# Optimization experiments

Measured on AMD Instinct MI355X. Metric: run time of the kernel, lower is better.

The kernel has to match this reference:

```python
import jax, jax.numpy as jnp
import numpy as np

B, L, D = 256, 256, 128          # batch, max_len, embedding_dim
H = W = 16                       # H=int(sqrt(L)), W=L//H
N, CBD = 128, 1024               # embedding_num, code_book_dim = N*8 = D*8
BETA = 0.25
BN_EPS = 1e-3                    # tf.layers.batch_normalization default


def _conv(x, w, b):
    return jax.lax.conv_general_dilated(x, w, (1, 1), 'VALID',
        dimension_numbers=('NHWC', 'HWIO', 'NHWC')) + b


def _convT(x, w, b):
    return jax.lax.conv_transpose(x, w, (1, 1), 'VALID',
        dimension_numbers=('NHWC', 'HWIO', 'NHWC')) + b


def _bn(x, g, b):
    # inference-mode BN with moving_mean=0, moving_var=1 (tf.layers default training=False)
    return g * (x * (1.0 / np.sqrt(1.0 + BN_EPS))) + b


def setup_inputs() -> dict:
    key = jax.random.key(0)
    ks = jax.random.split(key, 24)
    rn = lambda k, s, sc=0.05: (jax.random.normal(k, s, dtype=jnp.float32) * sc)
    inp = {
        'x': jax.random.normal(ks[0], (B, L, D), dtype=jnp.float32),
        'mask': jnp.ones((B, L), dtype=jnp.float32),
        'code_book': jax.random.normal(ks[1], (N, CBD), dtype=jnp.float32),
        # encoder: conv2d k=2 valid, channels D -> 2D -> 4D -> 8D
        'ew1': rn(ks[2], (2, 2, D, 2 * D)), 'eb1': jnp.zeros((2 * D,), jnp.float32),
        'eg1': jnp.ones((2 * D,), jnp.float32), 'ebt1': jnp.zeros((2 * D,), jnp.float32),
        'ew2': rn(ks[3], (2, 2, 2 * D, 4 * D)), 'eb2': jnp.zeros((4 * D,), jnp.float32),
        'eg2': jnp.ones((4 * D,), jnp.float32), 'ebt2': jnp.zeros((4 * D,), jnp.float32),
        'ew3': rn(ks[4], (2, 2, 4 * D, 8 * D)), 'eb3': jnp.zeros((8 * D,), jnp.float32),
        # decoder: conv2d_transpose k=2 valid, channels 8D -> 4D -> 2D -> D
        'dw1': rn(ks[5], (2, 2, 8 * D, 4 * D)), 'db1': jnp.zeros((4 * D,), jnp.float32),
        'dg1': jnp.ones((4 * D,), jnp.float32), 'dbt1': jnp.zeros((4 * D,), jnp.float32),
        'dw2': rn(ks[6], (2, 2, 4 * D, 2 * D)), 'db2': jnp.zeros((2 * D,), jnp.float32),
        'dg2': jnp.ones((2 * D,), jnp.float32), 'dbt2': jnp.zeros((2 * D,), jnp.float32),
        'dw3': rn(ks[7], (2, 2, 2 * D, D)), 'db3': jnp.zeros((D,), jnp.float32),
    }
    return inp


def reference(x, mask, code_book,
              ew1, eb1, eg1, ebt1, ew2, eb2, eg2, ebt2, ew3, eb3,
              dw1, db1, dg1, dbt1, dw2, db2, dg2, dbt2, dw3, db3):
    # ---- encoder (conv branch) ----
    xi = x.reshape(-1, H, W, D)                                   # [B,16,16,D]
    h = jax.nn.relu(_bn(_conv(xi, ew1, eb1), eg1, ebt1))          # [B,15,15,2D]
    h = jax.nn.relu(_bn(_conv(h, ew2, eb2), eg2, ebt2))           # [B,14,14,4D]
    x_encode = _conv(h, ew3, eb3)                                 # [B,13,13,8D]

    # ---- VQ codebook lookup (get_quantized) ----
    flat = x_encode.reshape(-1, CBD)                              # [B*169, CBD]
    dist = (jnp.sum(flat ** 2, axis=1, keepdims=True)
            + jnp.sum(code_book ** 2, axis=1)
            - 2.0 * flat @ code_book.T)                           # [B*169, N]
    idx = jnp.argmin(dist, axis=1)
    quantized = code_book[idx].reshape(x_encode.shape)            # gather == one_hot @ code_book

    # ---- straight-through + decoder ----
    ste = x_encode + jax.lax.stop_gradient(quantized - x_encode)
    h = jax.nn.relu(_bn(_convT(ste, dw1, db1), dg1, dbt1))        # [B,14,14,4D]
    h = jax.nn.relu(_bn(_convT(h, dw2, db2), dg2, dbt2))          # [B,15,15,2D]
    vq = _convT(h, dw3, db3)                                      # [B,16,16,D]
    vq_x = vq.reshape(-1, L, D)

    vq_mean = jnp.sum(vq_x, axis=1) / jnp.sum(mask, axis=-1, keepdims=True)

    recon = jnp.mean((x - vq_x) ** 2)
    vq_l = jnp.mean((quantized - jax.lax.stop_gradient(x_encode)) ** 2)
    commit = jnp.mean((x_encode - jax.lax.stop_gradient(quantized)) ** 2)
    vqvae_loss = recon + vq_l + BETA * commit
    return (vq_mean, vq_x, x_encode, quantized, vqvae_loss)
```

## Files before the change

### kernel.cpp

```cpp
#include <hip/hip_runtime.h>
#include <math.h>

typedef float f4 __attribute__((ext_vector_type(4)));
typedef short s8 __attribute__((ext_vector_type(8)));

#define WS_FLOATS 66000000L
__device__ float g_fallback[WS_FLOATS];

__device__ __forceinline__ f4 ldg4(const float* p) { return *(const f4*)p; }

__device__ __forceinline__ unsigned short bfr(float x) {
    unsigned int u = __float_as_uint(x);
    u += 0x7fffu + ((u >> 16) & 1u);
    return (unsigned short)(u >> 16);
}
__device__ __forceinline__ float bff(unsigned short h) {
    return __uint_as_float(((unsigned int)h) << 16);
}
__device__ __forceinline__ s8 z8() { s8 z = {0,0,0,0,0,0,0,0}; return z; }

__device__ __forceinline__ void split8(const f4& x0, const f4& x1, s8& hi, s8& lo) {
#pragma unroll
    for (int e = 0; e < 4; ++e) {
        unsigned short h0 = bfr(x0[e]);
        hi[e] = (short)h0; lo[e] = (short)bfr(x0[e] - bff(h0));
        unsigned short h1 = bfr(x1[e]);
        hi[e + 4] = (short)h1; lo[e + 4] = (short)bfr(x1[e] - bff(h1));
    }
}

__device__ __forceinline__ void tpose64(const float* __restrict__ src,
                                        short* __restrict__ hi,
                                        short* __restrict__ lo,
                                        int K, int N, int tileId, int tid)
{
    __shared__ float ld[64][65];
    const int nt = N >> 6;
    const int k0 = (tileId / nt) << 6, n0 = (tileId % nt) << 6;
#pragma unroll
    for (int i = 0; i < 16; ++i) {
        int idx = tid + (i << 8);
        int r = idx >> 6, c = idx & 63;
        ld[r][c] = src[(long)(k0 + r) * N + n0 + c];
    }
    __syncthreads();
#pragma unroll
    for (int i = 0; i < 16; ++i) {
        int idx = tid + (i << 8);
        int nr = idx >> 6, kc = idx & 63;
        float x = ld[kc][nr];
        unsigned short h = bfr(x);
        long o = (long)(n0 + nr) * K + k0 + kc;
        hi[o] = (short)h;
        if (lo) lo[o] = (short)bfr(x - bff(h));
    }
}

__global__ __launch_bounds__(256)
void tpose_all(const float* __restrict__ ew1, const float* __restrict__ ew2,
               const float* __restrict__ ew3, const float* __restrict__ dw1,
               const float* __restrict__ dw2, const float* __restrict__ dw3,
               const float* __restrict__ cb,
               short* __restrict__ ewt1h, short* __restrict__ ewt1l,
               short* __restrict__ ewt2h, short* __restrict__ ewt2l,
               short* __restrict__ ewt3h,
               short* __restrict__ dwt1Th, short* __restrict__ dwt1Tl,
               short* __restrict__ dwt2h, short* __restrict__ dwt3h,
               short* __restrict__ cbh, short* __restrict__ cbl,
               float* __restrict__ zbuf)
{
    int b = blockIdx.x, t = threadIdx.x;
    if (b < 32) {
        tpose64(ew1, ewt1h, ewt1l, 512, 256, b, t);
    } else if (b < 160) {
        tpose64(ew2, ewt2h, ewt2l, 1024, 512, b - 32, t);
    } else if (b < 672) {
        tpose64(ew3, ewt3h, nullptr, 2048, 1024, b - 160, t);
    } else if (b < 1184) {
        int r = b - 672; int tt = r >> 7; int tile = r & 127;
        tpose64(dw1 + (long)tt * 524288, dwt1Th + (long)tt * 524288,
                dwt1Tl + (long)tt * 524288, 1024, 512, tile, t);
    } else if (b < 1312) {
        tpose64(dw2, dwt2h, nullptr, 2048, 256, b - 1184, t);
    } else if (b < 1344) {
        tpose64(dw3, dwt3h, nullptr, 1024, 128, b - 1312, t);
    } else if (b < 1856) {
        int i = (b - 1344) * 256 + t;
        float x = cb[i]; unsigned short h = bfr(x);
        cbh[i] = (short)h; cbl[i] = (short)bfr(x - bff(h));
    } else {
#pragma unroll
        for (int q = 0; q < 8; ++q) zbuf[t + 256 * q] = 0.f;
    }
}

__global__ __launch_bounds__(256)
void tposeP1(const float* __restrict__ p1, short* __restrict__ hi,
             short* __restrict__ lo)
{
    tpose64(p1, hi, lo, 2048, 128, blockIdx.x, threadIdx.x);
}

template<int EPI>
__global__ __launch_bounds__(512, 2)
void gemm256(const short* __restrict__ aSrc, const short* __restrict__ wHi,
             const float* __restrict__ bias, const float* __restrict__ gamma,
             const float* __restrict__ beta, void* __restrict__ oHi,
             double* __restrict__ sacc, const short* __restrict__ zsrc,
             int IH, int IW, int OHOW, int OW, int N, int K, int off,
             int ntShift, float bns)
{
    extern __shared__ short smem[];

    const int tid = threadIdx.x;
    const int w = tid >> 6;
    const int l = tid & 63;
    const int lr = l >> 3;
    const int lc = l & 7;
    const int fr = l & 15, fq = l >> 4;
    const int wm = (w >> 2) * 128;
    const int wn = (w & 3) * 64;

    int m0, n0;
    {
        const int nwg = gridDim.x;
        const int bid = blockIdx.x;
        const int q = nwg >> 3, r = nwg & 7;
        const int xcd = bid & 7, c = bid >> 3;
        const int wg = (xcd < r ? xcd * (q + 1) : r * (q + 1) + (xcd - r) * q) + c;
        const int NTm1 = (1 << ntShift) - 1;
        m0 = (wg >> ntShift) * 256;
        n0 = (wg & NTm1) * 256;
    }

    int bOff[4], oiA[4], ojA[4], bRowB[4];
#pragma unroll
    for (int i = 0; i < 4; ++i) {
        int row = (w << 5) + (i << 3) + lr;
        int m = m0 + row;
        int b = m / OHOW; int rem = m - b * OHOW;
        oiA[i] = rem / OW; ojA[i] = rem - oiA[i] * OW;
        bOff[i] = b * IH * IW;
        bRowB[i] = (n0 + row) * K;
    }
    const int swz = (lc ^ lr) << 3;

    auto stage = [&](int sel, int kc) {
        short* Ab = smem + sel * 16384;
        short* Bb = smem + 32768 + sel * 16384;
        const int t = kc >> 9;
        const int ci = (kc & 511) + swz;
        const int di = (t >> 1) + off, dj = (t & 1) + off;
#pragma unroll
        for (int i = 0; i < 4; ++i) {
            int ii = oiA[i] + di, jj = ojA[i] + dj;
            bool v = (ii >= 0) && (ii < IH) && (jj >= 0) && (jj < IW);
            const short* sA = v ? aSrc + (long)(bOff[i] + ii * IW + jj) * 512 + ci
                                : zsrc + (l << 3);
            __builtin_amdgcn_global_load_lds(
                (const __attribute__((address_space(1))) void*)sA,
                (__attribute__((address_space(3))) void*)(Ab + (((w << 5) + (i << 3)) * 64)),
                16, 0, 0);
            const short* sB = wHi + bRowB[i] + kc + swz;
            __builtin_amdgcn_global_load_lds(
                (const __attribute__((address_space(1))) void*)sB,
                (__attribute__((address_space(3))) void*)(Bb + (((w << 5) + (i << 3)) * 64)),
                16, 0, 0);
        }
    };

    f4 acc[8][4];
#pragma unroll
    for (int a = 0; a < 8; ++a)
#pragma unroll
        for (int b = 0; b < 4; ++b) acc[a][b] = (f4){0.f, 0.f, 0.f, 0.f};

    const int NT = K >> 6;
    stage(0, 0);
    stage(1, 64);

    for (int t = 0; t < NT; ++t) {
        const int sel = t & 1;
        const short* Ab = smem + sel * 16384;
        const short* Bb = smem + 32768 + sel * 16384;

        if (t < NT - 1) asm volatile("s_waitcnt vmcnt(8)" ::: "memory");
        else            asm volatile("s_waitcnt vmcnt(0)" ::: "memory");
        __builtin_amdgcn_s_barrier();
        __builtin_amdgcn_sched_barrier(0);

        s8 af[8], bf[4];
#pragma unroll
        for (int mf = 0; mf < 8; ++mf) {
            int row = wm + mf * 16 + fr;
            int c = fq ^ (row & 7);
            af[mf] = *(const s8*)&Ab[row * 64 + (c << 3)];
        }
#pragma unroll
        for (int nf = 0; nf < 4; ++nf) {
            int row = wn + nf * 16 + fr;
            int c = fq ^ (row & 7);
            bf[nf] = *(const s8*)&Bb[row * 64 + (c << 3)];
        }
        asm volatile("s_waitcnt lgkmcnt(0)" ::: "memory");
        __builtin_amdgcn_sched_barrier(0);
        __builtin_amdgcn_s_setprio(1);
#pragma unroll
        for (int mf = 0; mf < 8; ++mf)
#pragma unroll
            for (int nf = 0; nf < 4; ++nf)
                acc[mf][nf] = __builtin_amdgcn_mfma_f32_16x16x32_bf16(
                    af[mf], bf[nf], acc[mf][nf], 0, 0, 0);
        __builtin_amdgcn_s_setprio(0);

#pragma unroll
        for (int mf = 0; mf < 8; ++mf) {
            int row = wm + mf * 16 + fr;
            int c = (4 + fq) ^ (row & 7);
            af[mf] = *(const s8*)&Ab[row * 64 + (c << 3)];
        }
#pragma unroll
        for (int nf = 0; nf < 4; ++nf) {
            int row = wn + nf * 16 + fr;
            int c = (4 + fq) ^ (row & 7);
            bf[nf] = *(const s8*)&Bb[row * 64 + (c << 3)];
        }
        asm volatile("s_waitcnt lgkmcnt(0)" ::: "memory");
        __builtin_amdgcn_sched_barrier(0);
        __builtin_amdgcn_s_barrier();
        __builtin_amdgcn_sched_barrier(0);
        if (t + 2 < NT) stage(sel, (t + 2) << 6);

        __builtin_amdgcn_s_setprio(1);
#pragma unroll
        for (int mf = 0; mf < 8; ++mf)
#pragma unroll
            for (int nf = 0; nf < 4; ++nf)
                acc[mf][nf] = __builtin_amdgcn_mfma_f32_16x16x32_bf16(
                    af[mf], bf[nf], acc[mf][nf], 0, 0, 0);
        __builtin_amdgcn_s_setprio(0);
    }

    if (EPI == 3) {
        float bi[4];
#pragma unroll
        for (int nf = 0; nf < 4; ++nf) bi[nf] = bias[n0 + wn + nf * 16 + fr];
        double tsum = 0.0;
#pragma unroll
        for (int mf = 0; mf < 8; ++mf)
#pragma unroll
            for (int j = 0; j < 4; ++j) {
                long gm = m0 + wm + mf * 16 + fq * 4 + j;
                float* orow = (float*)oHi + gm * (long)N + n0;
#pragma unroll
                for (int nf = 0; nf < 4; ++nf) {
                    float v = acc[mf][nf][j] + bi[nf];
                    orow[wn + nf * 16 + fr] = v;
                    tsum += (double)v * v;
                }
            }
        __syncthreads();
        double* rd = (double*)smem;
        rd[tid] = tsum; __syncthreads();
        for (int h = 256; h; h >>= 1) {
            if (tid < h) rd[tid] += rd[tid + h];
            __syncthreads();
        }
        if (tid == 0) atomicAdd(sacc, rd[0]);
    } else {
        float bi[4], ga[4], be[4];
#pragma unroll
        for (int nf = 0; nf < 4; ++nf) {
            int col = n0 + wn + nf * 16 + fr;
            bi[nf] = bias[col]; ga[nf] = gamma[col]; be[nf] = beta[col];
        }
#pragma unroll
        for (int mf = 0; mf < 8; ++mf)
#pragma unroll
            for (int j = 0; j < 4; ++j) {
                long gm = m0 + wm + mf * 16 + fq * 4 + j;
                short* orow = (short*)oHi + gm * (long)N + n0;
#pragma unroll
                for (int nf = 0; nf < 4; ++nf) {
                    float v = ga[nf] * ((acc[mf][nf][j] + bi[nf]) * bns) + be[nf];
                    orow[wn + nf * 16 + fr] = (short)bfr(fmaxf(v, 0.f));
                }
            }
    }
}

template<int SPLIT, int ASRC, int EPI, int OUTF>
__global__ __launch_bounds__(256, 2)
void mfma_conv(const void* __restrict__ aHi, const void* __restrict__ aLo,
               const short* __restrict__ wHi, const short* __restrict__ wLo,
               const float* __restrict__ bias, const float* __restrict__ gamma,
               const float* __restrict__ beta,
               void* __restrict__ oHi, void* __restrict__ oLo,
               int* __restrict__ idxo,
               const float* __restrict__ xref, float* __restrict__ colsum,
               double* __restrict__ sacc,
               int IH, int IW, int Cin, int cinShift, int OHOW, int OW,
               int N, int K, int off, int ntShift, float bns)
{
    constexpr int PL = 128 * 64;
    constexpr int NPL = (SPLIT == 1) ? 3 : 4;
    __shared__ short smem[NPL * PL];
    short* Ah = smem;
    short* Al  = smem + PL;
    short* BhS = smem + 2 * PL;
    short* BlS = smem + 3 * PL;

    const int tid = threadIdx.x;
    const int lane = tid & 63, wid = tid >> 6;
    const int fr = lane & 15, fq = lane >> 4;
    const int wm = (wid >> 1) * 64, wn = (wid & 1) * 64;

    int m0, n0;
    {
        const int nwg = gridDim.x;
        const int bid = blockIdx.x;
        const int q = nwg >> 3, r = nwg & 7;
        const int xcd = bid & 7, c = bid >> 3;
        const int wg = (xcd < r ? xcd * (q + 1) : r * (q + 1) + (xcd - r) * q) + c;
        const int NTm1 = (1 << ntShift) - 1;
        m0 = (wg >> ntShift) * 128;
        n0 = (wg & NTm1) * 128;
    }

    const int sr = tid >> 1;
    const int skh = (tid & 1) << 5;

    long tapOff[4]; bool tv[4];
    {
        int m = m0 + sr;
        int b = m / OHOW; int rem = m - b * OHOW;
        int oi = rem / OW; int oj = rem - oi * OW;
#pragma unroll
        for (int t = 0; t < 4; ++t) {
            int ii = oi + (t >> 1) + off, jj = oj + (t & 1) + off;
            bool v = (ii >= 0) && (ii < IH) && (jj >= 0) && (jj < IW);
            tv[t] = v;
            tapOff[t] = ((long)b * IH + (v ? ii : 0)) * IW + (v ? jj : 0);
        }
    }

    f4 acc[4][4];
#pragma unroll
    for (int a = 0; a < 4; ++a)
#pragma unroll
        for (int b = 0; b < 4; ++b) acc[a][b] = (f4){0.f, 0.f, 0.f, 0.f};

    const short* wHrow = wHi + (long)(n0 + sr) * K;
    const short* wLrow = (SPLIT == 2) ? (wLo + (long)(n0 + sr) * K) : nullptr;

    const int swzW = (sr & 7) << 3;
    const int sbase = sr * 64;

    s8 rah[4], ral[4], rbh[4], rbl[4];
    f4 rax0[4], rax1[4];

    auto LOADREGS = [&](int kc) {
        const int kk = kc + skh;
        const int t = kk >> cinShift;
        const int ci = kk & (Cin - 1);
        const bool v = tv[t];
        if (ASRC == 0) {
            const float* p = (const float*)aHi + tapOff[t] * Cin + ci;
#pragma unroll
            for (int q = 0; q < 4; ++q) {
                rax0[q] = v ? ldg4(p + 8 * q) : (f4){0.f,0.f,0.f,0.f};
                rax1[q] = v ? ldg4(p + 8 * q + 4) : (f4){0.f,0.f,0.f,0.f};
            }
        } else if (ASRC == 1) {
            const short* ph = (const short*)aHi + tapOff[t] * Cin + ci;
            const short* pl = (const short*)aLo + tapOff[t] * Cin + ci;
#pragma unroll
            for (int q = 0; q < 4; ++q) {
                rah[q] = v ? *(const s8*)(ph + 8 * q) : z8();
                ral[q] = v ? *(const s8*)(pl + 8 * q) : z8();
            }
        } else {
            const short* ph = (const short*)aHi + tapOff[t] * Cin + ci;
#pragma unroll
            for (int q = 0; q < 4; ++q) rah[q] = v ? *(const s8*)(ph + 8 * q) : z8();
        }
        if (SPLIT == 2) {
#pragma unroll
            for (int q = 0; q < 4; ++q) {
                rbh[q] = *(const s8*)(wHrow + kc + skh + 8 * q);
                rbl[q] = *(const s8*)(wLrow + kc + skh + 8 * q);
            }
        }
    };

    auto STORE = [&]() {
        if (ASRC == 0) {
#pragma unroll
            for (int q = 0; q < 4; ++q) split8(rax0[q], rax1[q], rah[q], ral[q]);
        }
#pragma unroll
        for (int q = 0; q < 4; ++q) {
            int kx = (skh + 8 * q) ^ swzW;
            *(s8*)&Ah[sbase + kx] = rah[q];
            if (SPLIT == 2) {
                *(s8*)&Al[sbase + kx]  = ral[q];
                *(s8*)&BhS[sbase + kx] = rbh[q];
                *(s8*)&BlS[sbase + kx] = rbl[q];
            }
        }
    };

    auto stageB = [&](int bsel, int kc2) {
        short* bb = smem + (1 + bsel) * PL;
        const int rr0 = wid << 5;
#pragma unroll
        for (int i = 0; i < 4; ++i) {
            const int r = rr0 + 8 * i + (lane >> 3);
            const int c = lane & 7;
            const short* src = wHi + (long)(n0 + r) * K + kc2 + 8 * (c ^ (r & 7));
            __builtin_amdgcn_global_load_lds(
                (const __attribute__((address_space(1))) void*)src,
                (__attribute__((address_space(3))) void*)(bb + (rr0 + 8 * i) * 64),
                16, 0, 0);
        }
    };

    int bcur = 0;
    LOADREGS(0);
    if (SPLIT == 1) stageB(0, 0);

    for (int kc = 0; kc < K; kc += 64) {
        if (SPLIT == 1) {
            asm volatile("s_waitcnt lgkmcnt(0)" ::: "memory");
            __builtin_amdgcn_s_barrier();
            STORE();
            if (kc + 64 < K) {
                stageB(bcur ^ 1, kc + 64);
                asm volatile("s_waitcnt vmcnt(4)" ::: "memory");
            } else {
                asm volatile("s_waitcnt vmcnt(0)" ::: "memory");
            }
            __builtin_amdgcn_sched_barrier(0);
            asm volatile("s_waitcnt lgkmcnt(0)" ::: "memory");
            __builtin_amdgcn_s_barrier();
        } else {
            __syncthreads();
            STORE();
            __syncthreads();
        }
        if (kc + 64 < K) LOADREGS(kc + 64);

        const short* Bc = (SPLIT == 1) ? (smem + (1 + bcur) * PL) : BhS;

        __builtin_amdgcn_s_setprio(1);
#pragma unroll
        for (int ks = 0; ks < 2; ++ks) {
            const int colk = ks * 32 + fq * 8;
            s8 afh[4], afl[4], bfh[4], bfl[4];
#pragma unroll
            for (int mf = 0; mf < 4; ++mf) {
                int ar = wm + mf * 16 + fr;
                int ai = ar * 64 + (colk ^ ((ar & 7) << 3));
                afh[mf] = *(const s8*)&Ah[ai];
                if (SPLIT == 2) afl[mf] = *(const s8*)&Al[ai];
            }
#pragma unroll
            for (int nf = 0; nf < 4; ++nf) {
                int br = wn + nf * 16 + fr;
                int bi2 = br * 64 + (colk ^ ((br & 7) << 3));
                bfh[nf] = *(const s8*)&Bc[bi2];
                if (SPLIT == 2) bfl[nf] = *(const s8*)&BlS[bi2];
            }
#pragma unroll
            for (int mf = 0; mf < 4; ++mf)
#pragma unroll
                for (int nf = 0; nf < 4; ++nf) {
                    acc[mf][nf] = __builtin_amdgcn_mfma_f32_16x16x32_bf16(
                        afh[mf], bfh[nf], acc[mf][nf], 0, 0, 0);
                    if (SPLIT == 2) {
                        acc[mf][nf] = __builtin_amdgcn_mfma_f32_16x16x32_bf16(
                            afh[mf], bfl[nf], acc[mf][nf], 0, 0, 0);
                        acc[mf][nf] = __builtin_amdgcn_mfma_f32_16x16x32_bf16(
                            afl[mf], bfh[nf], acc[mf][nf], 0, 0, 0);
                    }
                }
        }
        __builtin_amdgcn_s_setprio(0);
        bcur ^= 1;
    }

    if (EPI == 2) {
        __syncthreads();
        float* pbv = (float*)smem;
        int*   piv = (int*)((float*)smem + 256);
        float cnv[4];
#pragma unroll
        for (int nf = 0; nf < 4; ++nf) cnv[nf] = bias[n0 + wn + nf * 16 + fr];
#pragma unroll
        for (int mf = 0; mf < 4; ++mf)
#pragma unroll
            for (int j = 0; j < 4; ++j) {
                float best = 3.4e38f; int bi = 0;
#pragma unroll
                for (int nf = 0; nf < 4; ++nf) {
                    float d = cnv[nf] - 2.0f * acc[mf][nf][j];
                    int col = wn + nf * 16 + fr;
                    if (d < best) { best = d; bi = col; }
                }
#pragma unroll
                for (int sh = 1; sh <= 8; sh <<= 1) {
                    float ov = __shfl_xor(best, sh, 64);
                    int ob = __shfl_xor(bi, sh, 64);
                    if (ov < best || (ov == best && ob < bi)) { best = ov; bi = ob; }
                }
                if (fr == 0) {
                    int r = wm + mf * 16 + fq * 4 + j;
                    pbv[(wid & 1) * 128 + r] = best;
                    piv[(wid & 1) * 128 + r] = bi;
                }
            }
        __syncthreads();
        double win = 0.0;
        if (tid < 128) {
            float b0 = pbv[tid], b1 = pbv[128 + tid];
            int i0 = piv[tid], i1 = piv[128 + tid];
            idxo[m0 + tid] = (b1 < b0) ? i1 : i0;
            win = (double)((b1 < b0) ? b1 : b0);
        }
        __syncthreads();
        double* rd = (double*)smem;
        rd[tid] = win; __syncthreads();
        for (int h = 128; h; h >>= 1) {
            if (tid < h) rd[tid] += rd[tid + h];
            __syncthreads();
        }
        if (tid == 0) atomicAdd(sacc, rd[0]);
        return;
    }

    float bi[4], ga[4], be[4];
#pragma unroll
    for (int nf = 0; nf < 4; ++nf) {
        int col = n0 + wn + nf * 16 + fr;
        bi[nf] = bias[col];
        if (EPI == 1) { ga[nf] = gamma[col]; be[nf] = beta[col]; }
    }
    double tsum = 0.0;
    float csum[4] = {0.f, 0.f, 0.f, 0.f};
#pragma unroll
    for (int mf = 0; mf < 4; ++mf)
#pragma unroll
        for (int j = 0; j < 4; ++j) {
            long gm = m0 + wm + mf * 16 + fq * 4 + j;
#pragma unroll
            for (int nf = 0; nf < 4; ++nf) {
                int col = n0 + wn + nf * 16 + fr;
                float vv = acc[mf][nf][j] + bi[nf];
                if (EPI == 1) {
                    vv = ga[nf] * (vv * bns) + be[nf];
                    vv = fmaxf(vv, 0.f);
                }
                long o = gm * (long)N + col;
                if (OUTF == 0) {
                    ((float*)oHi)[o] = vv;
                } else if (OUTF == 2) {
                    ((short*)oHi)[o] = (short)bfr(vv);
                } else {
                    unsigned short h = bfr(vv);
                    ((short*)oHi)[o] = (short)h;
                    ((short*)oLo)[o] = (short)bfr(vv - bff(h));
                }
                if (EPI == 3) tsum += (double)vv * vv;
                if (EPI == 4) {
                    float d = vv - xref[o];
                    tsum += (double)d * d;
                    csum[nf] += vv;
                }
            }
        }
    if (EPI == 4) {
        int bb128 = (m0 >> 8) * 128;
#pragma unroll
        for (int nf = 0; nf < 4; ++nf)
            atomicAdd(&colsum[bb128 + n0 + wn + nf * 16 + fr], csum[nf]);
    }
    if (EPI == 3 || EPI == 4) {
        __syncthreads();
        double* rd = (double*)smem;
        rd[tid] = tsum; __syncthreads();
        for (int h = 128; h; h >>= 1) {
            if (tid < h) rd[tid] += rd[tid + h];
            __syncthreads();
        }
        if (tid == 0) atomicAdd(sacc, rd[0]);
    }
}

__global__ void code_bias(const float* __restrict__ cb, const float* __restrict__ eb3,
                          float* __restrict__ bias2)
{
    int c = blockIdx.x * 4 + (threadIdx.x >> 6);
    int lane = threadIdx.x & 63;
    if (c >= 128) return;
    const f4* p = (const f4*)(cb + (long)c * 1024);
    const f4* e = (const f4*)eb3;
    float s2 = 0.f, su = 0.f;
#pragma unroll
    for (int q = 0; q < 4; ++q) {
        f4 v = p[q * 64 + lane];
        f4 w = e[q * 64 + lane];
        s2 += (v[0]*v[0] + v[1]*v[1]) + (v[2]*v[2] + v[3]*v[3]);
        su += (v[0]*w[0] + v[1]*w[1]) + (v[2]*w[2] + v[3]*w[3]);
    }
#pragma unroll
    for (int sh = 32; sh; sh >>= 1) {
        s2 += __shfl_xor(s2, sh, 64);
        su += __shfl_xor(su, sh, 64);
    }
    if (lane == 0) bias2[c] = s2 - 2.f * su;
}

__global__ __launch_bounds__(256)
void d1_gather(const float* __restrict__ CD, const int* __restrict__ idx,
               const float* __restrict__ db1, const float* __restrict__ dg1,
               const float* __restrict__ dbt1, short* __restrict__ out, float bns)
{
    int m = blockIdx.x * 4 + (threadIdx.x >> 6);
    int lane = threadIdx.x & 63;
    if (m >= 50176) return;
    int b = m / 196, rem = m - b * 196;
    int oi = rem / 14, oj = rem - oi * 14;
    float2 acc[4];
#pragma unroll
    for (int q = 0; q < 4; ++q) acc[q] = make_float2(0.f, 0.f);
#pragma unroll
    for (int t = 0; t < 4; ++t) {
        int ii = oi - 1 + (t >> 1), jj = oj - 1 + (t & 1);
        if (ii >= 0 && ii < 13 && jj >= 0 && jj < 13) {
            int c = idx[(b * 13 + ii) * 13 + jj];
            const float2* p = (const float2*)(CD + ((long)c * 2048 + t * 512));
#pragma unroll
            for (int q = 0; q < 4; ++q) {
                float2 v = p[lane + 64 * q];
                acc[q].x += v.x; acc[q].y += v.y;
            }
        }
    }
#pragma unroll
    for (int q = 0; q < 4; ++q) {
        int n = 2 * (lane + 64 * q);
        float v0 = fmaxf(dg1[n]     * ((acc[q].x + db1[n])     * bns) + dbt1[n],     0.f);
        float v1 = fmaxf(dg1[n + 1] * ((acc[q].y + db1[n + 1]) * bns) + dbt1[n + 1], 0.f);
        short2 s2v;
        s2v.x = (short)bfr(v0); s2v.y = (short)bfr(v1);
        ((short2*)out)[(long)m * 256 + lane + 64 * q] = s2v;
    }
}

__global__ void gather_rows(const float* __restrict__ cb, const int* __restrict__ idx,
                            float* __restrict__ q)
{
    int m = blockIdx.x;
    int c = idx[m];
    const f4* src = (const f4*)(cb + (long)c * 1024);
    f4* dst = (f4*)(q + (long)m * 1024);
    dst[threadIdx.x] = src[threadIdx.x];
}

__global__ void finalize2(const double* __restrict__ s, float* __restrict__ loss)
{
    if (threadIdx.x == 0)
        loss[0] = (float)(s[0] / 8388608.0 + 1.25 * ((s[1] + s[2]) / 44302336.0));
}

__global__ void vq_mean_fin(const float* __restrict__ colsum,
                            const float* __restrict__ mask, float* __restrict__ o)
{
    __shared__ float red[128];
    int b = blockIdx.x;
    int d = threadIdx.x;
    red[d] = mask[b * 256 + d] + mask[b * 256 + 128 + d];
    __syncthreads();
    for (int h = 64; h; h >>= 1) { if (d < h) red[d] += red[d + h]; __syncthreads(); }
    o[b * 128 + d] = colsum[b * 128 + d] / red[0];
}

extern "C" void kernel_launch(void* const* d_in, const int* in_sizes, int n_in,
                              void* d_out, int out_size, void* d_ws, size_t ws_size,
                              hipStream_t stream)
{
    const float* x    = (const float*)d_in[0];
    const float* mask = (const float*)d_in[1];
    const float* cb   = (const float*)d_in[2];
    const float* ew1 = (const float*)d_in[3];
    const float* eb1 = (const float*)d_in[4];
    const float* eg1 = (const float*)d_in[5];
    const float* ebt1= (const float*)d_in[6];
    const float* ew2 = (const float*)d_in[7];
    const float* eb2 = (const float*)d_in[8];
    const float* eg2 = (const float*)d_in[9];
    const float* ebt2= (const float*)d_in[10];
    const float* ew3 = (const float*)d_in[11];
    const float* eb3 = (const float*)d_in[12];
    const float* dw1 = (const float*)d_in[13];
    const float* db1 = (const float*)d_in[14];
    const float* dg1 = (const float*)d_in[15];
    const float* dbt1= (const float*)d_in[16];
    const float* dw2 = (const float*)d_in[17];
    const float* db2 = (const float*)d_in[18];
    const float* dg2 = (const float*)d_in[19];
    const float* dbt2= (const float*)d_in[20];
    const float* dw3 = (const float*)d_in[21];
    const float* db3 = (const float*)d_in[22];

    float* out = (float*)d_out;
    float* o_vqmean = out;
    float* o_vqx    = out + 32768;
    float* o_xe     = out + 8421376;
    float* o_q      = out + 52723712;
    float* o_loss   = out + 97026048;

    float* base;
    if (ws_size >= (size_t)WS_FLOATS * 4) {
        base = (float*)d_ws;
    } else {
        void* p = nullptr;
        hipGetSymbolAddress(&p, HIP_SYMBOL(g_fallback));
        base = (float*)p;
    }

    float* cur = base;
    short* h1h = (short*)cur; cur += 7372800;
    short* h1l = (short*)cur; cur += 7372800;
    short* h2h = (short*)cur; cur += 12845056;
    short* h2l = (short*)cur; cur += 12845056;
    short* d1o = (short*)cur; cur += 12845056;
    short* d2o = (short*)cur; cur += 7372800;
    short* ewt1h = (short*)cur; cur += 65536;
    short* ewt1l = (short*)cur; cur += 65536;
    short* ewt2h = (short*)cur; cur += 262144;
    short* ewt2l = (short*)cur; cur += 262144;
    short* ewt3h = (short*)cur; cur += 1048576;
    short* dwt1Th = (short*)cur; cur += 1048576;
    short* dwt1Tl = (short*)cur; cur += 1048576;
    short* dwt2h = (short*)cur; cur += 262144;
    short* dwt3h = (short*)cur; cur += 65536;
    short* cbh   = (short*)cur; cur += 65536;
    short* cbl   = (short*)cur; cur += 65536;
    float* P1raw = cur; cur += 262144;
    short* wvh   = (short*)cur; cur += 131072;
    short* wvl   = (short*)cur; cur += 131072;
    float* CDt   = cur; cur += 262144;
    float* bias2 = cur; cur += 128;
    float* zbuf  = cur; cur += 2048;
    int* idxb = (int*)cur; cur += 43264;
    float* colsum = cur; cur += 32768;
    double* sdbl = (double*)cur; cur += 16;

    const float bns = (float)(1.0 / sqrt(1.0 + 1e-3));

    hipFuncSetAttribute(reinterpret_cast<const void*>(&gemm256<3>),
                        hipFuncAttributeMaxDynamicSharedMemorySize, 131072);
    hipFuncSetAttribute(reinterpret_cast<const void*>(&gemm256<1>),
                        hipFuncAttributeMaxDynamicSharedMemorySize, 131072);

    hipMemsetAsync(colsum, 0, 32768 * sizeof(float), stream);
    hipMemsetAsync(sdbl, 0, 3 * sizeof(double), stream);
    tpose_all<<<1857, 256, 0, stream>>>(ew1, ew2, ew3, dw1, dw2, dw3, cb,
        ewt1h, ewt1l, ewt2h, ewt2l, ewt3h, dwt1Th, dwt1Tl, dwt2h, dwt3h,
        cbh, cbl, zbuf);
    code_bias<<<32, 256, 0, stream>>>(cb, eb3, bias2);

    mfma_conv<2, 0, 0, 0><<<16, 256, 0, stream>>>(
        ew3, nullptr, cbh, cbl, zbuf, nullptr, nullptr, P1raw, nullptr, nullptr,
        nullptr, nullptr, nullptr,
        2, 2050, 1024, 10, 2048, 2048, 128, 1024, 0, 0, bns);
    tposeP1<<<64, 256, 0, stream>>>(P1raw, wvh, wvl);
    mfma_conv<2, 0, 0, 0><<<16, 256, 0, stream>>>(
        cb, nullptr, dwt1Th, dwt1Tl, zbuf, nullptr, nullptr, CDt, nullptr, nullptr,
        nullptr, nullptr, nullptr,
        2, 130, 1024, 10, 128, 128, 2048, 1024, 0, 4, bns);

    mfma_conv<2, 0, 1, 1><<<900, 256, 0, stream>>>(
        x, nullptr, ewt1h, ewt1l, eb1, eg1, ebt1, h1h, h1l, nullptr,
        nullptr, nullptr, nullptr,
        16, 16, 128, 7, 225, 15, 256, 512, 0, 1, bns);
    mfma_conv<2, 1, 1, 1><<<1568, 256, 0, stream>>>(
        h1h, h1l, ewt2h, ewt2l, eb2, eg2, ebt2, h2h, h2l, nullptr,
        nullptr, nullptr, nullptr,
        15, 15, 256, 8, 196, 14, 512, 1024, 0, 2, bns);
    gemm256<3><<<676, 512, 131072, stream>>>(
        h2h, ewt3h, eb3, nullptr, nullptr, o_xe, sdbl + 1, (const short*)zbuf,
        14, 14, 169, 13, 1024, 2048, 0, 2, bns);

    mfma_conv<2, 1, 2, 0><<<338, 256, 0, stream>>>(
        h2h, h2l, wvh, wvl, bias2, nullptr, nullptr, nullptr, nullptr, idxb,
        nullptr, nullptr, sdbl + 2,
        14, 14, 512, 9, 169, 13, 128, 2048, 0, 0, bns);
    gather_rows<<<43264, 256, 0, stream>>>(cb, idxb, o_q);

    d1_gather<<<12544, 256, 0, stream>>>(CDt, idxb, db1, dg1, dbt1, d1o, bns);
    gemm256<1><<<225, 512, 131072, stream>>>(
        d1o, dwt2h, db2, dg2, dbt2, d2o, nullptr, (const short*)zbuf,
        14, 14, 225, 15, 256, 2048, -1, 0, bns);
    mfma_conv<1, 2, 4, 0><<<512, 256, 0, stream>>>(
        d2o, nullptr, dwt3h, nullptr, db3, nullptr, nullptr, o_vqx, nullptr, nullptr,
        x, colsum, sdbl + 0,
        15, 15, 256, 8, 256, 16, 128, 1024, -1, 0, bns);

    vq_mean_fin<<<256, 128, 0, stream>>>(colsum, mask, o_vqmean);
    finalize2<<<1, 64, 0, stream>>>(sdbl, o_loss);
}
```

Baseline: 883.8 us.

## Fuse codebook gather, bias, and loss finalize into neighboring kernels

```diff
diff --git a/kernel.cpp b/kernel.cpp
--- a/kernel.cpp
+++ b/kernel.cpp
@@ -60,14 +60,14 @@
 void tpose_all(const float* __restrict__ ew1, const float* __restrict__ ew2,
                const float* __restrict__ ew3, const float* __restrict__ dw1,
                const float* __restrict__ dw2, const float* __restrict__ dw3,
-               const float* __restrict__ cb,
+               const float* __restrict__ cb, const float* __restrict__ eb3,
                short* __restrict__ ewt1h, short* __restrict__ ewt1l,
                short* __restrict__ ewt2h, short* __restrict__ ewt2l,
                short* __restrict__ ewt3h,
                short* __restrict__ dwt1Th, short* __restrict__ dwt1Tl,
                short* __restrict__ dwt2h, short* __restrict__ dwt3h,
                short* __restrict__ cbh, short* __restrict__ cbl,
-               float* __restrict__ zbuf)
+               float* __restrict__ zbuf, float* __restrict__ bias2)
 {
     int b = blockIdx.x, t = threadIdx.x;
     if (b < 32) {
@@ -88,9 +88,30 @@
         int i = (b - 1344) * 256 + t;
         float x = cb[i]; unsigned short h = bfr(x);
         cbh[i] = (short)h; cbl[i] = (short)bfr(x - bff(h));
+    } else if (b < 1857) {
+#pragma unroll
+        for (int q = 0; q < 8; ++q) zbuf[t + 256 * q] = 0.f;
     } else {
-#pragma unroll
-        for (int q = 0; q < 8; ++q) zbuf[t + 256 * q] = 0.f;
+        int c = (b - 1857) * 4 + (t >> 6);
+        int lane = t & 63;
+        if (c < 128) {
+            const f4* p = (const f4*)(cb + (long)c * 1024);
+            const f4* e = (const f4*)eb3;
+            float s2 = 0.f, su = 0.f;
+#pragma unroll
+            for (int q = 0; q < 4; ++q) {
+                f4 v = p[q * 64 + lane];
+                f4 w = e[q * 64 + lane];
+                s2 += (v[0]*v[0] + v[1]*v[1]) + (v[2]*v[2] + v[3]*v[3]);
+                su += (v[0]*w[0] + v[1]*w[1]) + (v[2]*w[2] + v[3]*w[3]);
+            }
+#pragma unroll
+            for (int sh = 32; sh; sh >>= 1) {
+                s2 += __shfl_xor(s2, sh, 64);
+                su += __shfl_xor(su, sh, 64);
+            }
+            if (lane == 0) bias2[c] = s2 - 2.f * su;
+        }
     }
 }
 
@@ -493,6 +514,8 @@
         __syncthreads();
         float* pbv = (float*)smem;
         int*   piv = (int*)((float*)smem + 256);
+        int*   fidx = (int*)((float*)smem + 512);
+        double* rd = (double*)((float*)smem + 768);
         float cnv[4];
 #pragma unroll
         for (int nf = 0; nf < 4; ++nf) cnv[nf] = bias[n0 + wn + nf * 16 + fr];
@@ -524,17 +547,26 @@
         if (tid < 128) {
             float b0 = pbv[tid], b1 = pbv[128 + tid];
             int i0 = piv[tid], i1 = piv[128 + tid];
-            idxo[m0 + tid] = (b1 < b0) ? i1 : i0;
+            int sel = (b1 < b0) ? i1 : i0;
+            idxo[m0 + tid] = sel;
+            fidx[tid] = sel;
             win = (double)((b1 < b0) ? b1 : b0);
         }
         __syncthreads();
-        double* rd = (double*)smem;
         rd[tid] = win; __syncthreads();
         for (int h = 128; h; h >>= 1) {
             if (tid < h) rd[tid] += rd[tid + h];
             __syncthreads();
         }
         if (tid == 0) atomicAdd(sacc, rd[0]);
+        const float* cbf = xref;
+        float* oq = (float*)oHi;
+#pragma unroll 4
+        for (int r = 0; r < 128; ++r) {
+            int c = fidx[r];
+            f4 v = *(const f4*)&cbf[(long)c * 1024 + 4 * tid];
+            *(f4*)&oq[((long)(m0 + r)) * 1024 + 4 * tid] = v;
+        }
         return;
     }
 
@@ -596,30 +628,6 @@
     }
 }
 
-__global__ void code_bias(const float* __restrict__ cb, const float* __restrict__ eb3,
-                          float* __restrict__ bias2)
-{
-    int c = blockIdx.x * 4 + (threadIdx.x >> 6);
-    int lane = threadIdx.x & 63;
-    if (c >= 128) return;
-    const f4* p = (const f4*)(cb + (long)c * 1024);
-    const f4* e = (const f4*)eb3;
-    float s2 = 0.f, su = 0.f;
-#pragma unroll
-    for (int q = 0; q < 4; ++q) {
-        f4 v = p[q * 64 + lane];
-        f4 w = e[q * 64 + lane];
-        s2 += (v[0]*v[0] + v[1]*v[1]) + (v[2]*v[2] + v[3]*v[3]);
-        su += (v[0]*w[0] + v[1]*w[1]) + (v[2]*w[2] + v[3]*w[3]);
-    }
-#pragma unroll
-    for (int sh = 32; sh; sh >>= 1) {
-        s2 += __shfl_xor(s2, sh, 64);
-        su += __shfl_xor(su, sh, 64);
-    }
-    if (lane == 0) bias2[c] = s2 - 2.f * su;
-}
-
 __global__ __launch_bounds__(256)
 void d1_gather(const float* __restrict__ CD, const int* __restrict__ idx,
                const float* __restrict__ db1, const float* __restrict__ dg1,
@@ -657,24 +665,10 @@
     }
 }
 
-__global__ void gather_rows(const float* __restrict__ cb, const int* __restrict__ idx,
-                            float* __restrict__ q)
-{
-    int m = blockIdx.x;
-    int c = idx[m];
-    const f4* src = (const f4*)(cb + (long)c * 1024);
-    f4* dst = (f4*)(q + (long)m * 1024);
-    dst[threadIdx.x] = src[threadIdx.x];
-}
-
-__global__ void finalize2(const double* __restrict__ s, float* __restrict__ loss)
-{
-    if (threadIdx.x == 0)
-        loss[0] = (float)(s[0] / 8388608.0 + 1.25 * ((s[1] + s[2]) / 44302336.0));
-}
-
 __global__ void vq_mean_fin(const float* __restrict__ colsum,
-                            const float* __restrict__ mask, float* __restrict__ o)
+                            const float* __restrict__ mask,
+                            const double* __restrict__ s,
+                            float* __restrict__ o, float* __restrict__ loss)
 {
     __shared__ float red[128];
     int b = blockIdx.x;
@@ -683,6 +677,8 @@
     __syncthreads();
     for (int h = 64; h; h >>= 1) { if (d < h) red[d] += red[d + h]; __syncthreads(); }
     o[b * 128 + d] = colsum[b * 128 + d] / red[0];
+    if (b == 0 && d == 0)
+        loss[0] = (float)(s[0] / 8388608.0 + 1.25 * ((s[1] + s[2]) / 44302336.0));
 }
 
 extern "C" void kernel_launch(void* const* d_in, const int* in_sizes, int n_in,
@@ -766,10 +762,9 @@
 
     hipMemsetAsync(colsum, 0, 32768 * sizeof(float), stream);
     hipMemsetAsync(sdbl, 0, 3 * sizeof(double), stream);
-    tpose_all<<<1857, 256, 0, stream>>>(ew1, ew2, ew3, dw1, dw2, dw3, cb,
+    tpose_all<<<1889, 256, 0, stream>>>(ew1, ew2, ew3, dw1, dw2, dw3, cb, eb3,
         ewt1h, ewt1l, ewt2h, ewt2l, ewt3h, dwt1Th, dwt1Tl, dwt2h, dwt3h,
-        cbh, cbl, zbuf);
-    code_bias<<<32, 256, 0, stream>>>(cb, eb3, bias2);
+        cbh, cbl, zbuf, bias2);
 
     mfma_conv<2, 0, 0, 0><<<16, 256, 0, stream>>>(
         ew3, nullptr, cbh, cbl, zbuf, nullptr, nullptr, P1raw, nullptr, nullptr,
@@ -794,10 +789,9 @@
         14, 14, 169, 13, 1024, 2048, 0, 2, bns);
 
     mfma_conv<2, 1, 2, 0><<<338, 256, 0, stream>>>(
-        h2h, h2l, wvh, wvl, bias2, nullptr, nullptr, nullptr, nullptr, idxb,
-        nullptr, nullptr, sdbl + 2,
+        h2h, h2l, wvh, wvl, bias2, nullptr, nullptr, o_q, nullptr, idxb,
+        cb, nullptr, sdbl + 2,
         14, 14, 512, 9, 169, 13, 128, 2048, 0, 0, bns);
-    gather_rows<<<43264, 256, 0, stream>>>(cb, idxb, o_q);
 
     d1_gather<<<12544, 256, 0, stream>>>(CDt, idxb, db1, dg1, dbt1, d1o, bns);
     gemm256<1><<<225, 512, 131072, stream>>>(
@@ -808,6 +802,5 @@
         x, colsum, sdbl + 0,
         15, 15, 256, 8, 256, 16, 128, 1024, -1, 0, bns);
 
-    vq_mean_fin<<<256, 128, 0, stream>>>(colsum, mask, o_vqmean);
-    finalize2<<<1, 64, 0, stream>>>(sdbl, o_loss);
-}
+    vq_mean_fin<<<256, 128, 0, stream>>>(colsum, mask, sdbl, o_vqmean, o_loss);
+}
```

After: 878.3 us. Within noise of the previous version (-0.6%).
